# Performance work log

Measured on AMD Instinct MI355X. Metric: run time of the kernel, lower is better.

## Reference

```python
import jax, jax.numpy as jnp
import numpy as np

B, TQ, TK, E, H, DH = 4, 1024, 1024, 1024, 16, 64
EPS = 1e-5

def setup_inputs() -> dict:
    key = jax.random.key(0)
    ks = jax.random.split(key, 16)
    s = 0.02
    return {
        "x": jax.random.normal(ks[0], (B, TQ, E), jnp.float32),
        "encoder_out": jax.random.normal(ks[1], (B, TK, E), jnp.float32),
        "Q1w": jax.random.normal(ks[2], (H, DH, E), jnp.float32) * s,
        "Q1b": jax.random.normal(ks[3], (H, DH), jnp.float32) * s,
        "Q2w": jax.random.normal(ks[4], (H, DH, E), jnp.float32) * s,
        "Q2b": jax.random.normal(ks[5], (H, DH), jnp.float32) * s,
        "K1w": jax.random.normal(ks[6], (H, DH, E), jnp.float32) * s,
        "K1b": jax.random.normal(ks[7], (H, DH), jnp.float32) * s,
        "K2w": jax.random.normal(ks[8], (H, DH, E), jnp.float32) * s,
        "K2b": jax.random.normal(ks[9], (H, DH), jnp.float32) * s,
        "Vw": jax.random.normal(ks[10], (H, DH, E), jnp.float32) * s,
        "Vb": jax.random.normal(ks[11], (H, DH), jnp.float32) * s,
        "lam": jax.random.uniform(ks[12], (H,), jnp.float32, 0.5, 1.0),
        "gn_gamma": jnp.ones((H * DH,), jnp.float32),
        "gn_beta": jnp.zeros((H * DH,), jnp.float32),
        "out_w": jax.random.normal(ks[13], (E, H * DH), jnp.float32) * s,
        "out_b": jax.random.normal(ks[14], (E,), jnp.float32) * s,
    }

def _proj(inp, w, b):
    # inp: [B,T,E], w: [H,DH,E] -> [B,H,T,DH]
    return jnp.einsum('bte,hde->bhtd', inp, w) + b[None, :, None, :]

def reference(x, encoder_out, Q1w, Q1b, Q2w, Q2b, K1w, K1b, K2w, K2b, Vw, Vb,
              lam, gn_gamma, gn_beta, out_w, out_b):
    scale = 1.0 / jnp.sqrt(jnp.float32(DH))
    q1 = _proj(x, Q1w, Q1b)
    q2 = _proj(x, Q2w, Q2b)
    k1 = _proj(encoder_out, K1w, K1b)
    k2 = _proj(encoder_out, K2w, K2b)
    v = _proj(encoder_out, Vw, Vb)
    s1 = jnp.einsum('bhtd,bhsd->bhts', q1, k1) * scale  # [B,H,TQ,TK]
    s2 = jnp.einsum('bhtd,bhsd->bhts', q2, k2) * scale
    w = jax.nn.softmax(s1, axis=-1) - lam[None, :, None, None] * jax.nn.softmax(s2, axis=-1)
    out = jnp.einsum('bhts,bhsd->bhtd', w, v)  # [B,H,TQ,DH]
    # GroupNorm(num_groups=H, channels=H*DH) over [B,C,T]: per (B,H) stats over (T,DH)
    mu = jnp.mean(out, axis=(2, 3), keepdims=True)
    var = jnp.mean(jnp.square(out - mu), axis=(2, 3), keepdims=True)
    normed = (out - mu) * jax.lax.rsqrt(var + EPS)
    g = gn_gamma.reshape(H, DH)[None, :, None, :]
    b_ = gn_beta.reshape(H, DH)[None, :, None, :]
    normed = normed * g + b_
    y = normed.transpose(0, 2, 1, 3).reshape(B, TQ, H * DH)
    return y @ out_w.T + out_b
```

## Files before the change

kernel.cpp:

```cpp
#include <hip/hip_runtime.h>
#include <cmath>

typedef __bf16 bf16_t;
typedef bf16_t bf16x8 __attribute__((ext_vector_type(8)));
typedef bf16_t bf16x4 __attribute__((ext_vector_type(4)));
typedef float  f32x4  __attribute__((ext_vector_type(4)));

#define Bn  4
#define TQn 1024
#define TKn 1024
#define En  1024
#define Hn  16
#define DHn 64

static constexpr float EPSv = 1e-5f;
static constexpr float C_SCALE = 0.18033688011112042f;

#define GLDS16(g, l)                                                         \
    __builtin_amdgcn_global_load_lds(                                        \
        (const __attribute__((address_space(1))) void*)(g),                  \
        (__attribute__((address_space(3))) void*)(l), 16, 0, 0)

__global__ __launch_bounds__(256)
void cvt_all(const float* __restrict__ x, const float* __restrict__ enc,
             const float* __restrict__ q1w, const float* __restrict__ q2w,
             const float* __restrict__ k1w, const float* __restrict__ k2w,
             const float* __restrict__ vw,  const float* __restrict__ outw,
             bf16_t* __restrict__ xb, bf16_t* __restrict__ encb,
             bf16_t* __restrict__ wq, bf16_t* __restrict__ wkv,
             bf16_t* __restrict__ wob, float* __restrict__ stats)
{
    if (blockIdx.x == 0 && threadIdx.x < 128) stats[threadIdx.x] = 0.f;
    int idx = blockIdx.x * 256 + threadIdx.x;
    const float* src; bf16_t* dst;
    if      (idx <  524288) { src = x    + (size_t)idx * 8;              dst = xb   + (size_t)idx * 8; }
    else if (idx < 1048576) { src = enc  + (size_t)(idx -  524288) * 8;  dst = encb + (size_t)(idx -  524288) * 8; }
    else if (idx < 1179648) { src = q1w  + (size_t)(idx - 1048576) * 8;  dst = wq   + (size_t)(idx - 1048576) * 8; }
    else if (idx < 1310720) { src = q2w  + (size_t)(idx - 1179648) * 8;  dst = wq   + 1048576 + (size_t)(idx - 1179648) * 8; }
    else if (idx < 1441792) { src = k1w  + (size_t)(idx - 1310720) * 8;  dst = wkv  + (size_t)(idx - 1310720) * 8; }
    else if (idx < 1572864) { src = k2w  + (size_t)(idx - 1441792) * 8;  dst = wkv  + 1048576 + (size_t)(idx - 1441792) * 8; }
    else if (idx < 1703936) { src = vw   + (size_t)(idx - 1572864) * 8;  dst = wkv  + 2097152 + (size_t)(idx - 1572864) * 8; }
    else                    { src = outw + (size_t)(idx - 1703936) * 8;  dst = wob  + (size_t)(idx - 1703936) * 8; }
    float4 a = *(const float4*)src;
    float4 b = *(const float4*)(src + 4);
    bf16x8 o;
    o[0] = (bf16_t)a.x; o[1] = (bf16_t)a.y; o[2] = (bf16_t)a.z; o[3] = (bf16_t)a.w;
    o[4] = (bf16_t)b.x; o[5] = (bf16_t)b.y; o[6] = (bf16_t)b.z; o[7] = (bf16_t)b.w;
    *(bf16x8*)dst = o;
}

__global__ __launch_bounds__(256, 4)
void gemm_proj(const bf16_t* __restrict__ xb, const bf16_t* __restrict__ encb,
               const bf16_t* __restrict__ wq, const bf16_t* __restrict__ wkv,
               const float* __restrict__ q1b, const float* __restrict__ q2b,
               const float* __restrict__ k1b, const float* __restrict__ k2b,
               const float* __restrict__ vb,
               bf16_t* __restrict__ q12, bf16_t* __restrict__ k12v)
{
    __shared__ bf16_t sA[128 * 64];
    __shared__ bf16_t sB[128 * 64];
    const int tid = threadIdx.x;
    const int w = tid >> 6, lane = tid & 63;
    const int q = lane >> 4, r = lane & 15;
    const int wm = w & 1, wn = w >> 1;
    const int blockM = blockIdx.y * 128, blockN = blockIdx.x * 128;
    const int seg = blockN >> 10;
    const bf16_t* A = (seg < 2) ? xb : encb;
    const bf16_t* W = (seg < 2) ? (wq + (size_t)blockN * 1024)
                                : (wkv + (size_t)(blockN - 2048) * 1024);
    const float* bp = (seg == 0) ? q1b : (seg == 1) ? q2b :
                      (seg == 2) ? k1b : (seg == 3) ? k2b : vb;

    f32x4 acc[4][4];
#pragma unroll
    for (int i = 0; i < 4; ++i)
#pragma unroll
        for (int j = 0; j < 4; ++j) acc[i][j] = (f32x4){0.f, 0.f, 0.f, 0.f};

    for (int k0 = 0; k0 < 1024; k0 += 64) {
#pragma unroll
        for (int c = 0; c < 4; ++c) {
            const int s = c * 256 + tid;
            const int row = s >> 3;
            const int cg = (s & 7) ^ (row & 7);
            GLDS16(A + (size_t)(blockM + row) * 1024 + k0 + cg * 8, sA + c * 2048 + w * 512);
            GLDS16(W + (size_t)row * 1024 + k0 + cg * 8,            sB + c * 2048 + w * 512);
        }
        __syncthreads();
#pragma unroll
        for (int ks = 0; ks < 2; ++ks) {
            bf16x8 a[4], b[4];
#pragma unroll
            for (int i = 0; i < 4; ++i) {
                const int row = wm * 64 + i * 16 + r;
                const int g = (ks * 4 + q) ^ (row & 7);
                a[i] = *(const bf16x8*)&sA[row * 64 + g * 8];
            }
#pragma unroll
            for (int j = 0; j < 4; ++j) {
                const int row = wn * 64 + j * 16 + r;
                const int g = (ks * 4 + q) ^ (row & 7);
                b[j] = *(const bf16x8*)&sB[row * 64 + g * 8];
            }
#pragma unroll
            for (int i = 0; i < 4; ++i)
#pragma unroll
                for (int j = 0; j < 4; ++j)
                    acc[i][j] = __builtin_amdgcn_mfma_f32_16x16x32_bf16(a[i], b[j], acc[i][j], 0, 0, 0);
        }
        __syncthreads();
    }

    float bv[4];
#pragma unroll
    for (int j = 0; j < 4; ++j)
        bv[j] = bp[(blockN + wn * 64 + j * 16 + r) & 1023];

    bf16_t* rep = ((w & 2) ? sB : sA) + (w & 1) * 4096;
    if (seg < 4) {
#pragma unroll
        for (int i = 0; i < 4; ++i)
#pragma unroll
            for (int j = 0; j < 4; ++j)
#pragma unroll
                for (int e = 0; e < 4; ++e)
                    rep[(i * 16 + q * 4 + e) * 64 + j * 16 + r] = (bf16_t)(acc[i][j][e] + bv[j]);
    } else {
#pragma unroll
        for (int i = 0; i < 4; ++i)
#pragma unroll
            for (int j = 0; j < 4; ++j)
#pragma unroll
                for (int e = 0; e < 4; ++e)
                    rep[(j * 16 + r) * 64 + i * 16 + q * 4 + e] = (bf16_t)(acc[i][j][e] + bv[j]);
    }
    const int rrow = lane >> 3, rcol = (lane & 7) * 8;
#pragma unroll
    for (int t8 = 0; t8 < 8; ++t8) {
        const int row = t8 * 8 + rrow;
        bf16x8 v = *(const bf16x8*)&rep[row * 64 + rcol];
        if (seg < 4) {
            const int m = blockM + wm * 64 + row;
            const int bb = m >> 10, t = m & 1023;
            const int n = blockN + wn * 64 + rcol;
            const int h = (n >> 6) & 15, d = n & 63;
            bf16_t* dst = (seg < 2)
                ? q12  + ((size_t)(seg * 4 + bb) * 16 + h) * 65536 + (size_t)t * 64 + d
                : k12v + ((size_t)((seg - 2) * 4 + bb) * 16 + h) * 65536 + (size_t)t * 64 + d;
            *(bf16x8*)dst = v;
        } else {
            const int n = blockN + wn * 64 + row;
            const int h = (n >> 6) & 15, d = n & 63;
            const int m = blockM + wm * 64 + rcol;
            const int bb = m >> 10, t = m & 1023;
            *(bf16x8*)(k12v + ((size_t)(8 + bb) * 16 + h) * 65536 + (size_t)d * 1024 + t) = v;
        }
    }
}

__global__ __launch_bounds__(256, 4)
void gemm_out(const bf16_t* __restrict__ A, const bf16_t* __restrict__ W,
              const float* __restrict__ bias, float* __restrict__ C)
{
    __shared__ bf16_t sA[128 * 64];
    __shared__ bf16_t sB[128 * 64];
    const int tid = threadIdx.x;
    const int w = tid >> 6, lane = tid & 63;
    const int q = lane >> 4, r = lane & 15;
    const int wm = w & 1, wn = w >> 1;
    const int blockM = blockIdx.y * 128, blockN = blockIdx.x * 128;

    f32x4 acc[4][4];
#pragma unroll
    for (int i = 0; i < 4; ++i)
#pragma unroll
        for (int j = 0; j < 4; ++j) acc[i][j] = (f32x4){0.f, 0.f, 0.f, 0.f};

    for (int k0 = 0; k0 < 1024; k0 += 64) {
#pragma unroll
        for (int c = 0; c < 4; ++c) {
            const int s = c * 256 + tid;
            const int row = s >> 3;
            const int cg = (s & 7) ^ (row & 7);
            GLDS16(A + (size_t)(blockM + row) * 1024 + k0 + cg * 8, sA + c * 2048 + w * 512);
            GLDS16(W + (size_t)(blockN + row) * 1024 + k0 + cg * 8, sB + c * 2048 + w * 512);
        }
        __syncthreads();
#pragma unroll
        for (int ks = 0; ks < 2; ++ks) {
            bf16x8 a[4], b[4];
#pragma unroll
            for (int i = 0; i < 4; ++i) {
                const int row = wm * 64 + i * 16 + r;
                const int g = (ks * 4 + q) ^ (row & 7);
                a[i] = *(const bf16x8*)&sA[row * 64 + g * 8];
            }
#pragma unroll
            for (int j = 0; j < 4; ++j) {
                const int row = wn * 64 + j * 16 + r;
                const int g = (ks * 4 + q) ^ (row & 7);
                b[j] = *(const bf16x8*)&sB[row * 64 + g * 8];
            }
#pragma unroll
            for (int i = 0; i < 4; ++i)
#pragma unroll
                for (int j = 0; j < 4; ++j)
                    acc[i][j] = __builtin_amdgcn_mfma_f32_16x16x32_bf16(a[i], b[j], acc[i][j], 0, 0, 0);
        }
        __syncthreads();
    }

#pragma unroll
    for (int j = 0; j < 4; ++j) {
        const int n = blockN + wn * 64 + j * 16 + r;
        const float bv = bias[n];
#pragma unroll
        for (int i = 0; i < 4; ++i) {
            f32x4 v = acc[i][j];
#pragma unroll
            for (int e = 0; e < 4; ++e) {
                const int m = blockM + wm * 64 + i * 16 + q * 4 + e;
                C[(size_t)m * 1024 + n] = v[e] + bv;
            }
        }
    }
}

__global__ __launch_bounds__(512, 4)
void diff_attn_mfma(const bf16_t* __restrict__ q12, const bf16_t* __restrict__ k12v,
                    const float* __restrict__ lam, bf16_t* __restrict__ out,
                    float* __restrict__ stats)
{
    __shared__ bf16_t sK1[64 * 64];
    __shared__ bf16_t sK2[64 * 64];
    __shared__ bf16_t sVt[64 * 64];
    __shared__ bf16_t sP [8 * 2048];

    const int tid = threadIdx.x;
    const int w = tid >> 6, lane = tid & 63;
    const int q = lane >> 4, r = lane & 15;
    const int bh = blockIdx.x, qt = blockIdx.y;
    const float lamv = lam[bh & (Hn - 1)];

    bf16_t* sP1 = sP + w * 2048;
    bf16_t* sP2 = sP1 + 1024;

    const size_t HT = (size_t)TKn * DHn;
    const bf16_t* q1g = q12 + (size_t)bh * HT + ((size_t)qt * 128 + w * 16) * 64;
    const bf16_t* q2g = q1g + 64 * HT;
    const bf16_t* k1g = k12v + (size_t)bh * HT;
    const bf16_t* k2g = k1g + 64 * HT;
    const bf16_t* vg  = k12v + (size_t)(128 + bh) * HT;

    bf16x8 fQ1[2], fQ2[2];
#pragma unroll
    for (int ks = 0; ks < 2; ++ks) {
        fQ1[ks] = *(const bf16x8*)(q1g + (size_t)r * 64 + ks * 32 + q * 8);
        fQ2[ks] = *(const bf16x8*)(q2g + (size_t)r * 64 + ks * 32 + q * 8);
    }

    f32x4 O1[4], O2[4];
    float l1 = 0.f, l2 = 0.f;
#pragma unroll
    for (int j = 0; j < 4; ++j) { O1[j] = (f32x4){0.f,0.f,0.f,0.f}; O2[j] = (f32x4){0.f,0.f,0.f,0.f}; }

    const int srow = tid >> 3;
    const int scg  = (tid & 7) ^ (srow & 7);

    for (int st = 0; st < TKn / 64; ++st) {
        __syncthreads();
        GLDS16(k1g + (size_t)st * 4096 + srow * 64 + scg * 8, sK1 + w * 512);
        GLDS16(k2g + (size_t)st * 4096 + srow * 64 + scg * 8, sK2 + w * 512);
        GLDS16(vg + (size_t)srow * 1024 + st * 64 + scg * 8,  sVt + w * 512);
        __syncthreads();

#pragma unroll
        for (int stream = 0; stream < 2; ++stream) {
            const bf16_t* sK = stream ? sK2 : sK1;
            const bf16x8* fQ = stream ? fQ2 : fQ1;
            bf16_t* sPw = stream ? sP2 : sP1;

            f32x4 S[4];
#pragma unroll
            for (int i = 0; i < 4; ++i) S[i] = (f32x4){0.f,0.f,0.f,0.f};
#pragma unroll
            for (int ks = 0; ks < 2; ++ks) {
#pragma unroll
                for (int i = 0; i < 4; ++i) {
                    const int g = (ks * 4 + q) ^ (r & 7);
                    bf16x8 fK = *(const bf16x8*)&sK[(i * 16 + r) * 64 + g * 8];
                    S[i] = __builtin_amdgcn_mfma_f32_16x16x32_bf16(fK, fQ[ks], S[i], 0, 0, 0);
                }
            }
            float part = 0.f;
#pragma unroll
            for (int i = 0; i < 4; ++i) {
                bf16x4 pk;
#pragma unroll
                for (int e = 0; e < 4; ++e) {
                    const float p = __builtin_amdgcn_exp2f(S[i][e] * C_SCALE);
                    part += p;
                    pk[e] = (bf16_t)p;
                }
                const int sb = i * 16 + q * 4;
                const int g = (sb >> 3) ^ (r & 7);
                *(bf16x4*)&sPw[r * 64 + g * 8 + (sb & 7)] = pk;
            }
            if (stream) l2 += part; else l1 += part;
        }

#pragma unroll
        for (int ks = 0; ks < 2; ++ks) {
            const int g = (ks * 4 + q) ^ (r & 7);
            bf16x8 fP1 = *(const bf16x8*)&sP1[r * 64 + g * 8];
            bf16x8 fP2 = *(const bf16x8*)&sP2[r * 64 + g * 8];
#pragma unroll
            for (int j = 0; j < 4; ++j) {
                bf16x8 fV = *(const bf16x8*)&sVt[(j * 16 + r) * 64 + g * 8];
                O1[j] = __builtin_amdgcn_mfma_f32_16x16x32_bf16(fP1, fV, O1[j], 0, 0, 0);
                O2[j] = __builtin_amdgcn_mfma_f32_16x16x32_bf16(fP2, fV, O2[j], 0, 0, 0);
            }
        }
    }

    l1 += __shfl_xor(l1, 16); l1 += __shfl_xor(l1, 32);
    l2 += __shfl_xor(l2, 16); l2 += __shfl_xor(l2, 32);

    bf16_t* op = out + ((size_t)bh * TQn + (size_t)qt * 128 + w * 16) * DHn;
    float ssum = 0.f, ssq = 0.f;
#pragma unroll
    for (int e = 0; e < 4; ++e) {
        const int t_l = q * 4 + e;
        const float inv1 = 1.0f / __shfl(l1, t_l);
        const float inv2 = lamv / __shfl(l2, t_l);
#pragma unroll
        for (int j = 0; j < 4; ++j) {
            const float o = O1[j][e] * inv1 - O2[j][e] * inv2;
            op[(size_t)t_l * 64 + j * 16 + r] = (bf16_t)o;
            ssum += o;
            ssq += o * o;
        }
    }
#pragma unroll
    for (int d = 1; d < 64; d <<= 1) {
        ssum += __shfl_xor(ssum, d);
        ssq  += __shfl_xor(ssq, d);
    }
    if (lane == 0) {
        atomicAdd(&stats[bh], ssum);
        atomicAdd(&stats[64 + bh], ssq);
    }
}

__global__ __launch_bounds__(256)
void gn_apply(const bf16_t* __restrict__ attn, const float* __restrict__ stats,
              const float* __restrict__ gamma, const float* __restrict__ beta,
              bf16_t* __restrict__ y)
{
    const int f = blockIdx.x * 256 + threadIdx.x;
    const int d8 = (f & 7) << 3;
    const int t  = (f >> 3) & 1023;
    const int bh = f >> 13;
    const int h  = bh & 15;
    const int b  = bh >> 4;
    const float s1 = stats[bh], s2 = stats[64 + bh];
    const float mu = s1 * (1.f / 65536.f);
    const float var = s2 * (1.f / 65536.f) - mu * mu;
    const float rstd = rsqrtf(var + EPSv);
    bf16x8 v = *(const bf16x8*)&attn[((size_t)bh << 16) + t * 64 + d8];
    const int c = h * 64 + d8;
    const float* gp = gamma + c;
    const float* bp = beta + c;
    bf16x8 o;
#pragma unroll
    for (int i = 0; i < 8; ++i)
        o[i] = (bf16_t)(((float)v[i] - mu) * rstd * gp[i] + bp[i]);
    *(bf16x8*)&y[((size_t)(b * 1024 + t)) * 1024 + c] = o;
}

extern "C" void kernel_launch(void* const* d_in, const int* in_sizes, int n_in,
                              void* d_out, int out_size, void* d_ws, size_t ws_size,
                              hipStream_t stream)
{
    const float* x    = (const float*)d_in[0];
    const float* enc  = (const float*)d_in[1];
    const float* Q1w  = (const float*)d_in[2];
    const float* Q1b  = (const float*)d_in[3];
    const float* Q2w  = (const float*)d_in[4];
    const float* Q2b  = (const float*)d_in[5];
    const float* K1w  = (const float*)d_in[6];
    const float* K1b  = (const float*)d_in[7];
    const float* K2w  = (const float*)d_in[8];
    const float* K2b  = (const float*)d_in[9];
    const float* Vw   = (const float*)d_in[10];
    const float* Vb   = (const float*)d_in[11];
    const float* lam  = (const float*)d_in[12];
    const float* gng  = (const float*)d_in[13];
    const float* gnb  = (const float*)d_in[14];
    const float* outw = (const float*)d_in[15];
    const float* outb = (const float*)d_in[16];
    float* out = (float*)d_out;

    bf16_t* xb   = (bf16_t*)d_ws;
    bf16_t* encb = xb   + 4194304;
    bf16_t* wq   = encb + 4194304;
    bf16_t* wkv  = wq   + 2097152;
    bf16_t* wob  = wkv  + 3145728;
    bf16_t* q12  = wob  + 1048576;
    bf16_t* k12v = q12  + 8388608;
    bf16_t* yb   = k12v + 12582912;
    bf16_t* attnb= yb   + 4194304;
    float*  stats= (float*)(attnb + 4194304);

    cvt_all<<<7168, 256, 0, stream>>>(x, enc, Q1w, Q2w, K1w, K2w, Vw, outw,
                                      xb, encb, wq, wkv, wob, stats);

    gemm_proj<<<dim3(40, 32), 256, 0, stream>>>(xb, encb, wq, wkv,
                                                Q1b, Q2b, K1b, K2b, Vb,
                                                q12, k12v);

    diff_attn_mfma<<<dim3(64, 8), 512, 0, stream>>>(q12, k12v, lam, attnb, stats);

    gn_apply<<<2048, 256, 0, stream>>>(attnb, stats, gng, gnb, yb);

    gemm_out<<<dim3(8, 32), 256, 0, stream>>>(yb, wob, outb, out);
}
```

Baseline: 268.8 us.

## Split attention warps across stream, key-half and query-half with LDS reduction

Reorganises the differential-attention kernel so each block handles 64 query rows. Its 8 warps are split by softmax stream, by key-tile half and by query half, and each warp computes a 32x32 score tile instead of a 16x64 one. Partial outputs and row sums are combined through shared memory in a serialized accumulation, and the result is written with vectorized bf16 stores. Per-block stats are reduced before a single atomic. The grid doubles to 1024 blocks to improve parallelism, at the cost of extra syncs, LDS reduction traffic and lower declared occupancy.

Measured after the change: 264.2 us. No clear change (-1.7%).

```diff
diff --git a/kernel.cpp b/kernel.cpp
--- a/kernel.cpp
+++ b/kernel.cpp
@@ -226,129 +226,180 @@
     }
 }
 
-__global__ __launch_bounds__(512, 4)
+__global__ __launch_bounds__(512, 2)
 void diff_attn_mfma(const bf16_t* __restrict__ q12, const bf16_t* __restrict__ k12v,
                     const float* __restrict__ lam, bf16_t* __restrict__ out,
                     float* __restrict__ stats)
 {
-    __shared__ bf16_t sK1[64 * 64];
-    __shared__ bf16_t sK2[64 * 64];
-    __shared__ bf16_t sVt[64 * 64];
-    __shared__ bf16_t sP [8 * 2048];
+    __shared__ __align__(16) bf16_t smem[22528];
 
     const int tid = threadIdx.x;
     const int w = tid >> 6, lane = tid & 63;
     const int q = lane >> 4, r = lane & 15;
+    const int strm  = w & 1;
+    const int shalf = (w >> 1) & 1;
+    const int thalf = w >> 2;
     const int bh = blockIdx.x, qt = blockIdx.y;
     const float lamv = lam[bh & (Hn - 1)];
 
-    bf16_t* sP1 = sP + w * 2048;
-    bf16_t* sP2 = sP1 + 1024;
+    bf16_t* sK1 = smem;
+    bf16_t* sK2 = smem + 4096;
+    bf16_t* sVt = smem + 8192;
+    bf16_t* sPw = smem + 12288 + w * 1280;
+    float*  out_s = (float*)(smem + 12288);
+    float*  lsh   = (float*)smem;
+    float*  sred  = (float*)(smem + 4096);
 
     const size_t HT = (size_t)TKn * DHn;
-    const bf16_t* q1g = q12 + (size_t)bh * HT + ((size_t)qt * 128 + w * 16) * 64;
-    const bf16_t* q2g = q1g + 64 * HT;
+    const bf16_t* qg  = q12 + ((size_t)strm * 64 + bh) * HT
+                      + ((size_t)qt * 64 + thalf * 32) * 64;
     const bf16_t* k1g = k12v + (size_t)bh * HT;
-    const bf16_t* k2g = k1g + 64 * HT;
+    const bf16_t* k2g = k12v + (size_t)(64 + bh) * HT;
     const bf16_t* vg  = k12v + (size_t)(128 + bh) * HT;
 
-    bf16x8 fQ1[2], fQ2[2];
-#pragma unroll
-    for (int ks = 0; ks < 2; ++ks) {
-        fQ1[ks] = *(const bf16x8*)(q1g + (size_t)r * 64 + ks * 32 + q * 8);
-        fQ2[ks] = *(const bf16x8*)(q2g + (size_t)r * 64 + ks * 32 + q * 8);
-    }
-
-    f32x4 O1[4], O2[4];
-    float l1 = 0.f, l2 = 0.f;
-#pragma unroll
-    for (int j = 0; j < 4; ++j) { O1[j] = (f32x4){0.f,0.f,0.f,0.f}; O2[j] = (f32x4){0.f,0.f,0.f,0.f}; }
-
-    const int srow = tid >> 3;
-    const int scg  = (tid & 7) ^ (srow & 7);
+    bf16x8 fQ[2][2];
+#pragma unroll
+    for (int nj = 0; nj < 2; ++nj)
+#pragma unroll
+        for (int ks = 0; ks < 2; ++ks)
+            fQ[nj][ks] = *(const bf16x8*)(qg + (size_t)(nj * 16 + r) * 64 + ks * 32 + q * 8);
+
+    f32x4 O[2][4];
+    float lpart[2] = {0.f, 0.f};
+#pragma unroll
+    for (int i = 0; i < 2; ++i)
+#pragma unroll
+        for (int j = 0; j < 4; ++j) O[i][j] = (f32x4){0.f, 0.f, 0.f, 0.f};
+
+    const int crow = tid >> 3;
+    const int ccg  = (tid & 7) ^ (crow & 7);
+    const bf16_t* sK = strm ? sK2 : sK1;
 
     for (int st = 0; st < TKn / 64; ++st) {
         __syncthreads();
-        GLDS16(k1g + (size_t)st * 4096 + srow * 64 + scg * 8, sK1 + w * 512);
-        GLDS16(k2g + (size_t)st * 4096 + srow * 64 + scg * 8, sK2 + w * 512);
-        GLDS16(vg + (size_t)srow * 1024 + st * 64 + scg * 8,  sVt + w * 512);
-        __syncthreads();
-
-#pragma unroll
-        for (int stream = 0; stream < 2; ++stream) {
-            const bf16_t* sK = stream ? sK2 : sK1;
-            const bf16x8* fQ = stream ? fQ2 : fQ1;
-            bf16_t* sPw = stream ? sP2 : sP1;
-
-            f32x4 S[4];
-#pragma unroll
-            for (int i = 0; i < 4; ++i) S[i] = (f32x4){0.f,0.f,0.f,0.f};
-#pragma unroll
-            for (int ks = 0; ks < 2; ++ks) {
-#pragma unroll
-                for (int i = 0; i < 4; ++i) {
-                    const int g = (ks * 4 + q) ^ (r & 7);
-                    bf16x8 fK = *(const bf16x8*)&sK[(i * 16 + r) * 64 + g * 8];
-                    S[i] = __builtin_amdgcn_mfma_f32_16x16x32_bf16(fK, fQ[ks], S[i], 0, 0, 0);
-                }
-            }
-            float part = 0.f;
-#pragma unroll
-            for (int i = 0; i < 4; ++i) {
+        GLDS16(k1g + (size_t)st * 4096 + crow * 64 + ccg * 8, smem + (size_t)tid * 8);
+        GLDS16(k2g + (size_t)st * 4096 + crow * 64 + ccg * 8, smem + 4096 + (size_t)tid * 8);
+        GLDS16(vg + (size_t)crow * 1024 + st * 64 + ccg * 8,  smem + 8192 + (size_t)tid * 8);
+        __syncthreads();
+
+        f32x4 S[2][2];
+#pragma unroll
+        for (int mi = 0; mi < 2; ++mi)
+#pragma unroll
+            for (int nj = 0; nj < 2; ++nj) S[mi][nj] = (f32x4){0.f, 0.f, 0.f, 0.f};
+#pragma unroll
+        for (int ks = 0; ks < 2; ++ks) {
+            bf16x8 fK[2];
+#pragma unroll
+            for (int mi = 0; mi < 2; ++mi) {
+                const int row = shalf * 32 + mi * 16 + r;
+                const int g = (ks * 4 + q) ^ (row & 7);
+                fK[mi] = *(const bf16x8*)&sK[row * 64 + g * 8];
+            }
+#pragma unroll
+            for (int mi = 0; mi < 2; ++mi)
+#pragma unroll
+                for (int nj = 0; nj < 2; ++nj)
+                    S[mi][nj] = __builtin_amdgcn_mfma_f32_16x16x32_bf16(fK[mi], fQ[nj][ks], S[mi][nj], 0, 0, 0);
+        }
+
+#pragma unroll
+        for (int nj = 0; nj < 2; ++nj) {
+            float ps = 0.f;
+#pragma unroll
+            for (int mi = 0; mi < 2; ++mi) {
                 bf16x4 pk;
 #pragma unroll
                 for (int e = 0; e < 4; ++e) {
-                    const float p = __builtin_amdgcn_exp2f(S[i][e] * C_SCALE);
-                    part += p;
+                    const float p = __builtin_amdgcn_exp2f(S[mi][nj][e] * C_SCALE);
+                    ps += p;
                     pk[e] = (bf16_t)p;
                 }
-                const int sb = i * 16 + q * 4;
-                const int g = (sb >> 3) ^ (r & 7);
-                *(bf16x4*)&sPw[r * 64 + g * 8 + (sb & 7)] = pk;
-            }
-            if (stream) l2 += part; else l1 += part;
-        }
-
-#pragma unroll
-        for (int ks = 0; ks < 2; ++ks) {
-            const int g = (ks * 4 + q) ^ (r & 7);
-            bf16x8 fP1 = *(const bf16x8*)&sP1[r * 64 + g * 8];
-            bf16x8 fP2 = *(const bf16x8*)&sP2[r * 64 + g * 8];
-#pragma unroll
-            for (int j = 0; j < 4; ++j) {
-                bf16x8 fV = *(const bf16x8*)&sVt[(j * 16 + r) * 64 + g * 8];
-                O1[j] = __builtin_amdgcn_mfma_f32_16x16x32_bf16(fP1, fV, O1[j], 0, 0, 0);
-                O2[j] = __builtin_amdgcn_mfma_f32_16x16x32_bf16(fP2, fV, O2[j], 0, 0, 0);
-            }
-        }
-    }
-
-    l1 += __shfl_xor(l1, 16); l1 += __shfl_xor(l1, 32);
-    l2 += __shfl_xor(l2, 16); l2 += __shfl_xor(l2, 32);
-
-    bf16_t* op = out + ((size_t)bh * TQn + (size_t)qt * 128 + w * 16) * DHn;
+                *(bf16x4*)&sPw[(nj * 16 + r) * 40 + mi * 16 + q * 4] = pk;
+            }
+            lpart[nj] += ps;
+        }
+
+        bf16x8 fV[4], fP[2];
+#pragma unroll
+        for (int j = 0; j < 4; ++j) {
+            const int d = j * 16 + r;
+            const int g = (shalf * 4 + q) ^ (d & 7);
+            fV[j] = *(const bf16x8*)&sVt[d * 64 + g * 8];
+        }
+#pragma unroll
+        for (int mt = 0; mt < 2; ++mt)
+            fP[mt] = *(const bf16x8*)&sPw[(mt * 16 + r) * 40 + q * 8];
+#pragma unroll
+        for (int mt = 0; mt < 2; ++mt)
+#pragma unroll
+            for (int j = 0; j < 4; ++j)
+                O[mt][j] = __builtin_amdgcn_mfma_f32_16x16x32_bf16(fP[mt], fV[j], O[mt][j], 0, 0, 0);
+    }
+
+    lpart[0] += __shfl_xor(lpart[0], 16); lpart[0] += __shfl_xor(lpart[0], 32);
+    lpart[1] += __shfl_xor(lpart[1], 16); lpart[1] += __shfl_xor(lpart[1], 32);
+    __syncthreads();
+    if (q == 0) {
+        lsh[w * 32 + r] = lpart[0];
+        lsh[w * 32 + 16 + r] = lpart[1];
+    }
+    __syncthreads();
+
+    float coef[2][4];
+#pragma unroll
+    for (int mt = 0; mt < 2; ++mt)
+#pragma unroll
+        for (int e = 0; e < 4; ++e) {
+            const int tl = mt * 16 + q * 4 + e;
+            const float lf = lsh[w * 32 + tl] + lsh[(w ^ 2) * 32 + tl];
+            coef[mt][e] = strm ? (-lamv / lf) : (1.f / lf);
+        }
+
+#pragma unroll
+    for (int k = 0; k < 4; ++k) {
+        if ((w & 3) == k) {
+#pragma unroll
+            for (int mt = 0; mt < 2; ++mt)
+#pragma unroll
+                for (int j = 0; j < 4; ++j)
+#pragma unroll
+                    for (int e = 0; e < 4; ++e) {
+                        const int row = thalf * 32 + mt * 16 + q * 4 + e;
+                        const int idx = row * 64 + j * 16 + r;
+                        const float val = O[mt][j][e] * coef[mt][e];
+                        if (k == 0) out_s[idx] = val;
+                        else        out_s[idx] += val;
+                    }
+        }
+        __syncthreads();
+    }
+
+    const int orow = tid >> 3, oc = (tid & 7) * 8;
+    f32x4 a = *(const f32x4*)&out_s[orow * 64 + oc];
+    f32x4 b = *(const f32x4*)&out_s[orow * 64 + oc + 4];
+    bf16x8 ov;
     float ssum = 0.f, ssq = 0.f;
 #pragma unroll
-    for (int e = 0; e < 4; ++e) {
-        const int t_l = q * 4 + e;
-        const float inv1 = 1.0f / __shfl(l1, t_l);
-        const float inv2 = lamv / __shfl(l2, t_l);
-#pragma unroll
-        for (int j = 0; j < 4; ++j) {
-            const float o = O1[j][e] * inv1 - O2[j][e] * inv2;
-            op[(size_t)t_l * 64 + j * 16 + r] = (bf16_t)o;
-            ssum += o;
-            ssq += o * o;
-        }
-    }
+    for (int i = 0; i < 4; ++i) {
+        ov[i] = (bf16_t)a[i];     ssum += a[i]; ssq += a[i] * a[i];
+        ov[4 + i] = (bf16_t)b[i]; ssum += b[i]; ssq += b[i] * b[i];
+    }
+    *(bf16x8*)&out[((size_t)bh * TQn + (size_t)qt * 64 + orow) * DHn + oc] = ov;
+
 #pragma unroll
     for (int d = 1; d < 64; d <<= 1) {
         ssum += __shfl_xor(ssum, d);
         ssq  += __shfl_xor(ssq, d);
     }
-    if (lane == 0) {
-        atomicAdd(&stats[bh], ssum);
-        atomicAdd(&stats[64 + bh], ssq);
+    if (lane == 0) { sred[w] = ssum; sred[8 + w] = ssq; }
+    __syncthreads();
+    if (tid == 0) {
+        float ts = 0.f, tq = 0.f;
+#pragma unroll
+        for (int i = 0; i < 8; ++i) { ts += sred[i]; tq += sred[8 + i]; }
+        atomicAdd(&stats[bh], ts);
+        atomicAdd(&stats[64 + bh], tq);
     }
 }
 
@@ -419,7 +470,7 @@
                                                 Q1b, Q2b, K1b, K2b, Vb,
                                                 q12, k12v);
 
-    diff_attn_mfma<<<dim3(64, 8), 512, 0, stream>>>(q12, k12v, lam, attnb, stats);
+    diff_attn_mfma<<<dim3(64, 16), 512, 0, stream>>>(q12, k12v, lam, attnb, stats);
 
     gn_apply<<<2048, 256, 0, stream>>>(attnb, stats, gng, gnb, yb);
 
```
